# Kernel tuning notes

Hardware: AMD Instinct MI355X
Metric: run time of the kernel (lower is better)

## Reference

```python
import jax, jax.numpy as jnp
import numpy as np

NUM_HEADS = 16
HEAD_DIM = 64
DIM = NUM_HEADS * HEAD_DIM
ROPE_BASE = 10000.0
EPS = 1e-6


def rotate_half(x):
    # pairs (x0,x1) -> (-x1, x0), interleaved on last dim
    x_even = x[..., ::2]
    x_odd = x[..., 1::2]
    return jnp.stack((-x_odd, x_even), axis=-1).reshape(x.shape)


def apply_rope(q, k, positions, base=ROPE_BASE):
    d = q.shape[-1]
    inv_freq = 1.0 / (base ** (jnp.arange(0, d, 2, dtype=jnp.float32) / d))
    angles = positions.astype(jnp.float32)[..., None] * inv_freq  # [B, L, d/2]
    cos = jnp.repeat(jnp.cos(angles), 2, axis=-1).astype(q.dtype)[:, None, :, :]  # [B,1,L,d]
    sin = jnp.repeat(jnp.sin(angles), 2, axis=-1).astype(q.dtype)[:, None, :, :]
    return q * cos + rotate_half(q) * sin, k * cos + rotate_half(k) * sin


def per_head_layernorm(x, weight):
    # x: [B, H, L, d]; weight: [H, d]; bias is zeros (qkv_bias=False)
    mu = jnp.mean(x, axis=-1, keepdims=True)
    var = jnp.mean(jnp.square(x - mu), axis=-1, keepdims=True)
    xn = (x - mu) * jax.lax.rsqrt(var + EPS)
    return xn * weight[None, :, None, :]


def setup_inputs() -> dict:
    key = jax.random.key(0)
    k1, k2, k3, k4, k5 = jax.random.split(key, 5)
    B, L = 2, 2048
    x = jax.random.normal(k1, (B, L, DIM), dtype=jnp.float32)
    mask = jnp.ones((B, L, L), dtype=bool)
    positions = jnp.broadcast_to(jnp.arange(L, dtype=jnp.int64 if jax.config.jax_enable_x64 else jnp.int32), (B, L))
    s = 1.0 / np.sqrt(DIM)
    W_qkv = jax.random.normal(k2, (DIM, 3 * DIM), dtype=jnp.float32) * s
    W_out = jax.random.normal(k3, (DIM, DIM), dtype=jnp.float32) * s
    qn_w = jnp.ones((NUM_HEADS, HEAD_DIM), dtype=jnp.float32)
    kn_w = jnp.ones((NUM_HEADS, HEAD_DIM), dtype=jnp.float32)
    return {"x": x, "mask": mask, "positions": positions,
            "W_qkv": W_qkv, "W_out": W_out, "qn_w": qn_w, "kn_w": kn_w}


def reference(x, mask, positions, W_qkv, W_out, qn_w, kn_w):
    B, L, D = x.shape
    scale = HEAD_DIM ** -0.5
    qkv = x @ W_qkv  # [B, L, 3D]
    qkv = qkv.reshape(B, L, 3, NUM_HEADS, HEAD_DIM)
    qkv = jnp.transpose(qkv, (2, 0, 3, 1, 4))  # [3, B, H, L, d]
    q, k, v = qkv[0], qkv[1], qkv[2]
    q = per_head_layernorm(q, qn_w)
    k = per_head_layernorm(k, kn_w)
    q, k = apply_rope(q, k, positions)
    attn = jnp.einsum('bhqd,bhkd->bhqk', q, k) * scale  # [B, H, L, L]
    attn = jnp.where(mask[:, None, :, :], attn, -jnp.inf)
    attn = jax.nn.softmax(attn, axis=-1)
    out = jnp.einsum('bhqk,bhkd->bhqd', attn, v)  # [B, H, L, d]
    out = jnp.transpose(out, (0, 2, 1, 3)).reshape(B, L, D)
    return out @ W_out
```

## Files before the change

### kernel.cpp

```cpp
#include <hip/hip_runtime.h>


typedef __bf16 bf16x8 __attribute__((ext_vector_type(8)));
typedef __bf16 bf16x2 __attribute__((ext_vector_type(2)));
typedef float f32x4 __attribute__((ext_vector_type(4)));

#define QSCALE 0.1803368802f

__device__ __forceinline__ float bf2f(unsigned short u) {
  unsigned int v = ((unsigned int)u) << 16;
  float f;
  __builtin_memcpy(&f, &v, 4);
  return f;
}
__device__ __forceinline__ unsigned short f2bf(float f) {
  unsigned int v;
  __builtin_memcpy(&v, &f, 4);
  v += 0x7fffu + ((v >> 16) & 1u);
  return (unsigned short)(v >> 16);
}
__device__ __forceinline__ unsigned short f2bf_hw(float f) {
  __bf16 h = (__bf16)f;
  unsigned short u;
  __builtin_memcpy(&u, &h, 2);
  return u;
}
__device__ __forceinline__ unsigned int pack2(float a, float b) {
  bf16x2 t;
  t[0] = (__bf16)a;
  t[1] = (__bf16)b;
  unsigned int u;
  __builtin_memcpy(&u, &t, 4);
  return u;
}
__device__ __forceinline__ void gl_lds16(const unsigned short* g, unsigned short* l) {
  __builtin_amdgcn_global_load_lds(
      (const __attribute__((address_space(1))) unsigned int*)g,
      (__attribute__((address_space(3))) unsigned int*)l, 16, 0, 0);
}

__global__ __launch_bounds__(256) void prep(
    const float* __restrict__ x, const float* __restrict__ W_qkv,
    const float* __restrict__ W_out, const int* __restrict__ positions,
    unsigned short* __restrict__ xb,
    unsigned short* __restrict__ Wt_qkv, unsigned short* __restrict__ Wt_out,
    float2* __restrict__ lut) {
  __shared__ float tile[64][65];
  const int bid = blockIdx.x, t = threadIdx.x;
  if (bid < 4096) {
    int i = (bid * 256 + t) * 4;
    float4 v = *reinterpret_cast<const float4*>(x + i);
    ushort4 o;
    o.x = f2bf(v.x); o.y = f2bf(v.y); o.z = f2bf(v.z); o.w = f2bf(v.w);
    *reinterpret_cast<ushort4*>(xb + i) = o;
    return;
  }
  if (bid >= 5120) {
    int idx = (bid - 5120) * 256 + t;
    int m = idx >> 5, p = idx & 31;
    float pos = (float)positions[m];
    float invf = __builtin_amdgcn_exp2f(-(float)(2 * p) * (13.2877124f / 64.0f));
    float rev = pos * invf * 0.15915494f;
    rev -= floorf(rev);
    lut[idx] = make_float2(__builtin_amdgcn_cosf(rev), __builtin_amdgcn_sinf(rev));
    return;
  }
  const float* W; unsigned short* Wt; int Nd, bn, bk;
  if (bid < 4864) {
    int id = bid - 4096; W = W_qkv; Wt = Wt_qkv; Nd = 3072; bn = id % 48; bk = id / 48;
  } else {
    int id = bid - 4864; W = W_out; Wt = Wt_out; Nd = 1024; bn = id % 16; bk = id / 16;
  }
  const int Kd = 1024;
#pragma unroll
  for (int i = 0; i < 16; i++) {
    int idx = i * 256 + t;
    int k = idx >> 6, n = idx & 63;
    tile[k][n] = W[(size_t)(bk * 64 + k) * Nd + bn * 64 + n];
  }
  __syncthreads();
#pragma unroll
  for (int i = 0; i < 16; i++) {
    int idx = i * 256 + t;
    int n = idx >> 6, k = idx & 63;
    Wt[(size_t)(bn * 64 + n) * Kd + bk * 64 + k] = f2bf(tile[k][n]);
  }
}

__global__ __launch_bounds__(256, 4) void gemm_qkv(
    const unsigned short* __restrict__ A,
    const unsigned short* __restrict__ Bt,
    const float* __restrict__ qn_w, const float* __restrict__ kn_w,
    const float2* __restrict__ lut,
    unsigned short* __restrict__ Qr,
    unsigned short* __restrict__ Kr,
    unsigned short* __restrict__ Vt, int K) {
  __shared__ __align__(16) unsigned short As[2][128 * 32];
  __shared__ __align__(16) unsigned short Bs[2][128 * 32];
  const int tid = threadIdx.x;
  const int lane = tid & 63, wid = tid >> 6;
  const int quad = lane >> 4, l16 = lane & 15;
  const int wr = wid >> 1, wc = wid & 1;
  const int bn = blockIdx.x, bm = blockIdx.y;
  const unsigned short* Ab = A + (size_t)bm * 128 * K;
  const unsigned short* Bb = Bt + (size_t)bn * 128 * K;

  f32x4 acc[4][4] = {};

  const int c0 = tid, c1 = tid + 256;
  const int ar0 = c0 >> 2, ag0 = ((c0 & 3) ^ ((ar0 >> 1) & 3)) * 8;
  const int ar1 = c1 >> 2, ag1 = ((c1 & 3) ^ ((ar1 >> 1) & 3)) * 8;

  gl_lds16(Ab + (size_t)ar0 * K + ag0, &As[0][c0 * 8]);
  gl_lds16(Ab + (size_t)ar1 * K + ag1, &As[0][c1 * 8]);
  gl_lds16(Bb + (size_t)ar0 * K + ag0, &Bs[0][c0 * 8]);
  gl_lds16(Bb + (size_t)ar1 * K + ag1, &Bs[0][c1 * 8]);

  const int iters = K >> 5;
  for (int it = 0; it < iters; it++) {
    const int cur = it & 1;
    __builtin_amdgcn_s_barrier();
    if (it + 1 < iters) {
      const int k0 = (it + 1) << 5, nb = cur ^ 1;
      gl_lds16(Ab + (size_t)ar0 * K + k0 + ag0, &As[nb][c0 * 8]);
      gl_lds16(Ab + (size_t)ar1 * K + k0 + ag1, &As[nb][c1 * 8]);
      gl_lds16(Bb + (size_t)ar0 * K + k0 + ag0, &Bs[nb][c0 * 8]);
      gl_lds16(Bb + (size_t)ar1 * K + k0 + ag1, &Bs[nb][c1 * 8]);
      __builtin_amdgcn_sched_barrier(0);
      asm volatile("s_waitcnt vmcnt(4)" ::: "memory");
    } else {
      __builtin_amdgcn_sched_barrier(0);
      asm volatile("s_waitcnt vmcnt(0)" ::: "memory");
    }
    __builtin_amdgcn_sched_barrier(0);
    __builtin_amdgcn_s_setprio(1);
    const unsigned short* Ac = As[cur];
    const unsigned short* Bc = Bs[cur];
    bf16x8 af[4], bfr[4];
#pragma unroll
    for (int i = 0; i < 4; i++) {
      int m = wr * 64 + i * 16 + l16;
      af[i] = *reinterpret_cast<const bf16x8*>(&Ac[m * 32 + ((quad ^ ((m >> 1) & 3)) * 8)]);
    }
#pragma unroll
    for (int j = 0; j < 4; j++) {
      int n = wc * 64 + j * 16 + l16;
      bfr[j] = *reinterpret_cast<const bf16x8*>(&Bc[n * 32 + ((quad ^ ((n >> 1) & 3)) * 8)]);
    }
#pragma unroll
    for (int i = 0; i < 4; i++)
#pragma unroll
      for (int j = 0; j < 4; j++)
        acc[i][j] = __builtin_amdgcn_mfma_f32_16x16x32_bf16(af[i], bfr[j], acc[i][j], 0, 0, 0);
    __builtin_amdgcn_s_setprio(0);
  }

  const int sec = bn >> 3;
  const int h = (bn & 7) * 2 + wc;
  const int b = bm >> 4;
  if (sec < 2) {
    const float* gw = sec ? kn_w : qn_w;
    unsigned short* dst = sec ? Kr : Qr;
    const float oscale = sec ? 1.0f : QSCALE;
    float w4[4];
#pragma unroll
    for (int j = 0; j < 4; j++) w4[j] = gw[h * 64 + j * 16 + l16];
#pragma unroll
    for (int i = 0; i < 4; i++)
#pragma unroll
      for (int r = 0; r < 4; r++) {
        int m = bm * 128 + wr * 64 + i * 16 + quad * 4 + r;
        int l = m & 2047;
        const float2* lrow = lut + m * 32;
        float2 cs4[4];
#pragma unroll
        for (int j = 0; j < 4; j++) cs4[j] = lrow[j * 8 + (l16 >> 1)];
        float sum = acc[i][0][r] + acc[i][1][r] + acc[i][2][r] + acc[i][3][r];
        float sq = acc[i][0][r] * acc[i][0][r] + acc[i][1][r] * acc[i][1][r] +
                   acc[i][2][r] * acc[i][2][r] + acc[i][3][r] * acc[i][3][r];
#pragma unroll
        for (int off = 1; off < 16; off <<= 1) {
          sum += __shfl_xor(sum, off);
          sq += __shfl_xor(sq, off);
        }
        float mu = sum * (1.0f / 64.0f);
        float var = sq * (1.0f / 64.0f) - mu * mu;
        float rs = rsqrtf(fmaxf(var, 0.0f) + 1e-6f);
#pragma unroll
        for (int j = 0; j < 4; j++) {
          float y = (acc[i][j][r] - mu) * rs * w4[j];
          float p = __shfl_xor(y, 1);
          float o = (l16 & 1) ? (y * cs4[j].x + p * cs4[j].y)
                              : (y * cs4[j].x - p * cs4[j].y);
          dst[((size_t)(b * 16 + h) * 2048 + l) * 64 + j * 16 + l16] = f2bf(o * oscale);
        }
      }
  } else {
#pragma unroll
    for (int i = 0; i < 4; i++) {
      int lp = (bm * 128 + wr * 64 + (i >> 1) * 32 + quad * 8 + (i & 1) * 4) & 2047;
#pragma unroll
      for (int j = 0; j < 4; j++) {
        int d = j * 16 + l16;
        uint2 v;
        v.x = pack2(acc[i][j][0], acc[i][j][1]);
        v.y = pack2(acc[i][j][2], acc[i][j][3]);
        *reinterpret_cast<uint2*>(&Vt[((size_t)(b * 16 + h) * 64 + d) * 2048 + lp]) = v;
      }
    }
  }
}

__global__ __launch_bounds__(256, 2) void attn_kernel(
    const unsigned short* __restrict__ Q,
    const unsigned short* __restrict__ K,
    const unsigned short* __restrict__ Vt,
    unsigned short* __restrict__ O) {
  __shared__ __align__(16) unsigned short Ks[2][2][64 * 64];
  __shared__ __align__(16) unsigned short Vs[2][2][64 * 64];

  int bid = blockIdx.x;
  int id = (bid & 7) * 64 + (bid >> 3);
  const int qt = id & 15; id >>= 4;
  const int h = id & 15;  const int b = id >> 4;
  const int tid = threadIdx.x;
  const int lane = tid & 63, wid = tid >> 6;
  const int half = wid >> 1, wg = wid & 1;
  const int quad = lane >> 4, l16 = lane & 15;

  const unsigned short* Qb = Q + (size_t)(b * 16 + h) * 2048 * 64;
  const unsigned short* Kb = K + (size_t)(b * 16 + h) * 2048 * 64;
  const unsigned short* Vb = Vt + (size_t)(b * 16 + h) * 64 * 2048;

  const int qbase = qt * 128 + wg * 64;
  bf16x8 qf[4][2];
#pragma unroll
  for (int g = 0; g < 4; g++)
#pragma unroll
    for (int d = 0; d < 2; d++)
      qf[g][d] = *reinterpret_cast<const bf16x8*>(
          &Qb[(size_t)(qbase + g * 16 + l16) * 64 + d * 32 + quad * 8]);

  bf16x8 ones8;
#pragma unroll
  for (int i = 0; i < 8; i++) ones8[i] = (__bf16)1.0f;

  f32x4 o[4][4] = {};
  f32x4 lacc[4] = {};

  const int ltid = tid & 127;
  int cs[4], rs[4], gsw[4];
#pragma unroll
  for (int j = 0; j < 4; j++) {
    cs[j] = ltid + j * 128;
    rs[j] = cs[j] >> 3;
    gsw[j] = ((cs[j] & 7) ^ (rs[j] & 7)) * 8;
  }
  const int kb0 = half * 1024;

#pragma unroll
  for (int j = 0; j < 4; j++)
    gl_lds16(&Kb[(size_t)(kb0 + rs[j]) * 64 + gsw[j]], &Ks[half][0][cs[j] * 8]);
#pragma unroll
  for (int j = 0; j < 4; j++)
    gl_lds16(&Vb[(size_t)rs[j] * 2048 + kb0 + gsw[j]], &Vs[half][0][cs[j] * 8]);

  for (int kt = 0; kt < 16; kt++) {
    const int cur = kt & 1;
    __builtin_amdgcn_s_barrier();
    if (kt + 1 < 16) {
      const int ko = kb0 + (kt + 1) * 64, nb = cur ^ 1;
#pragma unroll
      for (int j = 0; j < 4; j++)
        gl_lds16(&Kb[(size_t)(ko + rs[j]) * 64 + gsw[j]], &Ks[half][nb][cs[j] * 8]);
#pragma unroll
      for (int j = 0; j < 4; j++)
        gl_lds16(&Vb[(size_t)rs[j] * 2048 + ko + gsw[j]], &Vs[half][nb][cs[j] * 8]);
      __builtin_amdgcn_sched_barrier(0);
      asm volatile("s_waitcnt vmcnt(8)" ::: "memory");
    } else {
      __builtin_amdgcn_sched_barrier(0);
      asm volatile("s_waitcnt vmcnt(0)" ::: "memory");
    }
    __builtin_amdgcn_sched_barrier(0);
    const unsigned short* Kc = Ks[half][cur];
    const unsigned short* Vc = Vs[half][cur];

    __builtin_amdgcn_s_setprio(1);
    f32x4 s4[4][4] = {};
#pragma unroll
    for (int kg = 0; kg < 4; kg++) {
      int row = kg * 16 + l16;
      bf16x8 kf0 = *reinterpret_cast<const bf16x8*>(
          &Kc[row * 64 + ((quad ^ (row & 7)) * 8)]);
      bf16x8 kf1 = *reinterpret_cast<const bf16x8*>(
          &Kc[row * 64 + (((4 + quad) ^ (row & 7)) * 8)]);
#pragma unroll
      for (int g = 0; g < 4; g++) {
        s4[g][kg] = __builtin_amdgcn_mfma_f32_16x16x32_bf16(kf0, qf[g][0], s4[g][kg], 0, 0, 0);
        s4[g][kg] = __builtin_amdgcn_mfma_f32_16x16x32_bf16(kf1, qf[g][1], s4[g][kg], 0, 0, 0);
      }
    }
    union u32x4v { unsigned int u[4]; bf16x8 v; };
    u32x4v pa[4][2];
#pragma unroll
    for (int g = 0; g < 4; g++) {
      float pv[4][4];
#pragma unroll
      for (int kg = 0; kg < 4; kg++)
#pragma unroll
        for (int r = 0; r < 4; r++)
          pv[kg][r] = __builtin_amdgcn_exp2f(s4[g][kg][r]);
#pragma unroll
      for (int c = 0; c < 2; c++) {
        pa[g][c].u[0] = pack2(pv[c * 2][0], pv[c * 2][1]);
        pa[g][c].u[1] = pack2(pv[c * 2][2], pv[c * 2][3]);
        pa[g][c].u[2] = pack2(pv[c * 2 + 1][0], pv[c * 2 + 1][1]);
        pa[g][c].u[3] = pack2(pv[c * 2 + 1][2], pv[c * 2 + 1][3]);
        lacc[g] = __builtin_amdgcn_mfma_f32_16x16x32_bf16(pa[g][c].v, ones8, lacc[g], 0, 0, 0);
      }
    }
#pragma unroll
    for (int c = 0; c < 2; c++)
#pragma unroll
      for (int i = 0; i < 4; i++) {
        int row = i * 16 + l16;
        bf16x8 vfr = *reinterpret_cast<const bf16x8*>(
            &Vc[row * 64 + (((c * 4 + quad) ^ (row & 7)) * 8)]);
#pragma unroll
        for (int g = 0; g < 4; g++)
          o[g][i] = __builtin_amdgcn_mfma_f32_16x16x32_bf16(pa[g][c].v, vfr, o[g][i], 0, 0, 0);
      }
    __builtin_amdgcn_s_setprio(0);
  }

  __syncthreads();
  float* Om = (float*)&Ks[0][0][0];
  float* Lm = (float*)&Vs[0][0][0];
  if (half == 0) {
#pragma unroll
    for (int g = 0; g < 4; g++) {
#pragma unroll
      for (int i = 0; i < 4; i++)
#pragma unroll
        for (int r = 0; r < 4; r++)
          Om[(wg * 64 + g * 16 + quad * 4 + r) * 64 + i * 16 + l16] = o[g][i][r];
      if (l16 == 0) {
#pragma unroll
        for (int r = 0; r < 4; r++)
          Lm[wg * 64 + g * 16 + quad * 4 + r] = lacc[g][r];
      }
    }
  }
  __syncthreads();
  if (half == 1) {
#pragma unroll
    for (int g = 0; g < 4; g++) {
#pragma unroll
      for (int r = 0; r < 4; r++) {
        float lt = lacc[g][r] + Lm[wg * 64 + g * 16 + quad * 4 + r];
        float inv = 1.0f / lt;
        int q = qbase + g * 16 + quad * 4 + r;
#pragma unroll
        for (int i = 0; i < 4; i++) {
          float sum = o[g][i][r] + Om[(wg * 64 + g * 16 + quad * 4 + r) * 64 + i * 16 + l16];
          O[((size_t)(b * 2048 + q)) * 1024 + h * 64 + i * 16 + l16] = f2bf_hw(sum * inv);
        }
      }
    }
  }
}

__global__ __launch_bounds__(256) void gemm_out(
    const unsigned short* __restrict__ A,
    const unsigned short* __restrict__ Bt,
    float* __restrict__ C, int M, int N, int K) {
  __shared__ __align__(16) unsigned short As[2][128 * 64];
  __shared__ __align__(16) unsigned short Bs[2][64 * 64];
  const int tid = threadIdx.x;
  const int lane = tid & 63, wid = tid >> 6;
  const int quad = lane >> 4, l16 = lane & 15;
  const int bn = blockIdx.x, bm = blockIdx.y;
  const unsigned short* Ab = A + (size_t)bm * 128 * K;
  const unsigned short* Bb = Bt + (size_t)bn * 64 * K;

  f32x4 acc[2][4] = {};

  int arow[4], asrc[4];
#pragma unroll
  for (int t2 = 0; t2 < 4; t2++) {
    int s = t2 * 256 + tid;
    arow[t2] = s >> 3;
    asrc[t2] = (((s & 7) ^ (arow[t2] & 7)) * 8);
  }
  int brow[2], bsrc[2];
#pragma unroll
  for (int t2 = 0; t2 < 2; t2++) {
    int s = t2 * 256 + tid;
    brow[t2] = s >> 3;
    bsrc[t2] = (((s & 7) ^ (brow[t2] & 7)) * 8);
  }

#pragma unroll
  for (int t2 = 0; t2 < 4; t2++)
    gl_lds16(Ab + (size_t)arow[t2] * K + asrc[t2], &As[0][(t2 * 256 + tid) * 8]);
#pragma unroll
  for (int t2 = 0; t2 < 2; t2++)
    gl_lds16(Bb + (size_t)brow[t2] * K + bsrc[t2], &Bs[0][(t2 * 256 + tid) * 8]);

  const int iters = K >> 6;
  for (int it = 0; it < iters; it++) {
    const int cur = it & 1;
    __builtin_amdgcn_s_barrier();
    if (it + 1 < iters) {
      const int k0 = (it + 1) << 6, nb = cur ^ 1;
#pragma unroll
      for (int t2 = 0; t2 < 4; t2++)
        gl_lds16(Ab + (size_t)arow[t2] * K + k0 + asrc[t2], &As[nb][(t2 * 256 + tid) * 8]);
#pragma unroll
      for (int t2 = 0; t2 < 2; t2++)
        gl_lds16(Bb + (size_t)brow[t2] * K + k0 + bsrc[t2], &Bs[nb][(t2 * 256 + tid) * 8]);
      __builtin_amdgcn_sched_barrier(0);
      asm volatile("s_waitcnt vmcnt(6)" ::: "memory");
    } else {
      __builtin_amdgcn_sched_barrier(0);
      asm volatile("s_waitcnt vmcnt(0)" ::: "memory");
    }
    __builtin_amdgcn_sched_barrier(0);
    __builtin_amdgcn_s_setprio(1);
    const unsigned short* Ac = As[cur];
    const unsigned short* Bc = Bs[cur];
    bf16x8 af[2][2], bfr[4][2];
#pragma unroll
    for (int i = 0; i < 2; i++) {
      int m = wid * 32 + i * 16 + l16;
#pragma unroll
      for (int kk = 0; kk < 2; kk++)
        af[i][kk] = *reinterpret_cast<const bf16x8*>(
            &Ac[(m * 8 + ((kk * 4 + quad) ^ (m & 7))) * 8]);
    }
#pragma unroll
    for (int j = 0; j < 4; j++) {
      int n = j * 16 + l16;
#pragma unroll
      for (int kk = 0; kk < 2; kk++)
        bfr[j][kk] = *reinterpret_cast<const bf16x8*>(
            &Bc[(n * 8 + ((kk * 4 + quad) ^ (n & 7))) * 8]);
    }
#pragma unroll
    for (int kk = 0; kk < 2; kk++)
#pragma unroll
      for (int i = 0; i < 2; i++)
#pragma unroll
        for (int j = 0; j < 4; j++)
          acc[i][j] = __builtin_amdgcn_mfma_f32_16x16x32_bf16(af[i][kk], bfr[j][kk], acc[i][j], 0, 0, 0);
    __builtin_amdgcn_s_setprio(0);
  }
#pragma unroll
  for (int i = 0; i < 2; i++)
#pragma unroll
    for (int j = 0; j < 4; j++)
#pragma unroll
      for (int r = 0; r < 4; r++) {
        int m = bm * 128 + wid * 32 + i * 16 + quad * 4 + r;
        int n = bn * 64 + j * 16 + l16;
        C[(size_t)m * N + n] = acc[i][j][r];
      }
}

extern "C" void kernel_launch(void* const* d_in, const int* in_sizes, int n_in,
                              void* d_out, int out_size, void* d_ws, size_t ws_size,
                              hipStream_t stream) {
  (void)in_sizes; (void)n_in; (void)out_size; (void)ws_size;
  const float* x     = (const float*)d_in[0];
  const int*   pos   = (const int*)d_in[2];
  const float* W_qkv = (const float*)d_in[3];
  const float* W_out = (const float*)d_in[4];
  const float* qn_w  = (const float*)d_in[5];
  const float* kn_w  = (const float*)d_in[6];
  float*       out   = (float*)d_out;

  char* ws = (char*)d_ws;
  unsigned short* xb     = (unsigned short*)(ws);
  unsigned short* Qr     = (unsigned short*)(ws + 8388608);
  unsigned short* Kr     = (unsigned short*)(ws + 16777216);
  unsigned short* Vt     = (unsigned short*)(ws + 25165824);
  unsigned short* Wt_qkv = (unsigned short*)(ws + 33554432);
  unsigned short* Wt_out = (unsigned short*)(ws + 39845888);
  float2*         lut    = (float2*)(ws + 41943040);
  unsigned short* attn_o = xb;

  prep<<<5632, 256, 0, stream>>>(x, W_qkv, W_out, pos, xb, Wt_qkv, Wt_out, lut);
  gemm_qkv<<<dim3(24, 32), 256, 0, stream>>>(xb, Wt_qkv, qn_w, kn_w, lut, Qr, Kr, Vt, 1024);
  attn_kernel<<<512, 256, 0, stream>>>(Qr, Kr, Vt, attn_o);
  gemm_out<<<dim3(16, 32), 256, 0, stream>>>(attn_o, Wt_out, out, 4096, 1024, 1024);
}
```

Before: 197.8 us.

## Enlarge QKV GEMM tile to 256x256 with 512 threads and K-step 64

```diff
diff --git a/kernel.cpp b/kernel.cpp
--- a/kernel.cpp
+++ b/kernel.cpp
@@ -87,7 +87,7 @@
   }
 }
 
-__global__ __launch_bounds__(256, 4) void gemm_qkv(
+__global__ __launch_bounds__(512, 2) void gemm_qkv(
     const unsigned short* __restrict__ A,
     const unsigned short* __restrict__ Bt,
     const float* __restrict__ qn_w, const float* __restrict__ kn_w,
@@ -95,39 +95,50 @@
     unsigned short* __restrict__ Qr,
     unsigned short* __restrict__ Kr,
     unsigned short* __restrict__ Vt, int K) {
-  __shared__ __align__(16) unsigned short As[2][128 * 32];
-  __shared__ __align__(16) unsigned short Bs[2][128 * 32];
+  __shared__ __align__(16) unsigned short As[2][256 * 64];
+  __shared__ __align__(16) unsigned short Bs[2][256 * 64];
   const int tid = threadIdx.x;
   const int lane = tid & 63, wid = tid >> 6;
   const int quad = lane >> 4, l16 = lane & 15;
-  const int wr = wid >> 1, wc = wid & 1;
-  const int bn = blockIdx.x, bm = blockIdx.y;
-  const unsigned short* Ab = A + (size_t)bm * 128 * K;
-  const unsigned short* Bb = Bt + (size_t)bn * 128 * K;
-
-  f32x4 acc[4][4] = {};
-
-  const int c0 = tid, c1 = tid + 256;
-  const int ar0 = c0 >> 2, ag0 = ((c0 & 3) ^ ((ar0 >> 1) & 3)) * 8;
-  const int ar1 = c1 >> 2, ag1 = ((c1 & 3) ^ ((ar1 >> 1) & 3)) * 8;
-
-  gl_lds16(Ab + (size_t)ar0 * K + ag0, &As[0][c0 * 8]);
-  gl_lds16(Ab + (size_t)ar1 * K + ag1, &As[0][c1 * 8]);
-  gl_lds16(Bb + (size_t)ar0 * K + ag0, &Bs[0][c0 * 8]);
-  gl_lds16(Bb + (size_t)ar1 * K + ag1, &Bs[0][c1 * 8]);
-
-  const int iters = K >> 5;
+  const int wr = wid >> 2, wc = wid & 3;
+  int bid = blockIdx.x;
+  int id = (bid & 7) * 24 + (bid >> 3);
+  const int bn = id >> 4;
+  const int bm = id & 15;
+  const unsigned short* Ab = A + (size_t)bm * 256 * K;
+  const unsigned short* Bb = Bt + (size_t)bn * 256 * K;
+
+  f32x4 acc[8][4] = {};
+
+  int srow[4], ssw[4];
+#pragma unroll
+  for (int t2 = 0; t2 < 4; t2++) {
+    int s = t2 * 512 + tid;
+    srow[t2] = s >> 3;
+    ssw[t2] = (((s & 7) ^ (srow[t2] & 7)) * 8);
+  }
+
+#pragma unroll
+  for (int t2 = 0; t2 < 4; t2++)
+    gl_lds16(Ab + (size_t)srow[t2] * K + ssw[t2], &As[0][(t2 * 512 + tid) * 8]);
+#pragma unroll
+  for (int t2 = 0; t2 < 4; t2++)
+    gl_lds16(Bb + (size_t)srow[t2] * K + ssw[t2], &Bs[0][(t2 * 512 + tid) * 8]);
+
+  const int iters = K >> 6;
   for (int it = 0; it < iters; it++) {
     const int cur = it & 1;
     __builtin_amdgcn_s_barrier();
     if (it + 1 < iters) {
-      const int k0 = (it + 1) << 5, nb = cur ^ 1;
-      gl_lds16(Ab + (size_t)ar0 * K + k0 + ag0, &As[nb][c0 * 8]);
-      gl_lds16(Ab + (size_t)ar1 * K + k0 + ag1, &As[nb][c1 * 8]);
-      gl_lds16(Bb + (size_t)ar0 * K + k0 + ag0, &Bs[nb][c0 * 8]);
-      gl_lds16(Bb + (size_t)ar1 * K + k0 + ag1, &Bs[nb][c1 * 8]);
+      const int k0 = (it + 1) << 6, nb = cur ^ 1;
+#pragma unroll
+      for (int t2 = 0; t2 < 4; t2++)
+        gl_lds16(Ab + (size_t)srow[t2] * K + k0 + ssw[t2], &As[nb][(t2 * 512 + tid) * 8]);
+#pragma unroll
+      for (int t2 = 0; t2 < 4; t2++)
+        gl_lds16(Bb + (size_t)srow[t2] * K + k0 + ssw[t2], &Bs[nb][(t2 * 512 + tid) * 8]);
       __builtin_amdgcn_sched_barrier(0);
-      asm volatile("s_waitcnt vmcnt(4)" ::: "memory");
+      asm volatile("s_waitcnt vmcnt(8)" ::: "memory");
     } else {
       __builtin_amdgcn_sched_barrier(0);
       asm volatile("s_waitcnt vmcnt(0)" ::: "memory");
@@ -136,28 +147,34 @@
     __builtin_amdgcn_s_setprio(1);
     const unsigned short* Ac = As[cur];
     const unsigned short* Bc = Bs[cur];
-    bf16x8 af[4], bfr[4];
-#pragma unroll
-    for (int i = 0; i < 4; i++) {
-      int m = wr * 64 + i * 16 + l16;
-      af[i] = *reinterpret_cast<const bf16x8*>(&Ac[m * 32 + ((quad ^ ((m >> 1) & 3)) * 8)]);
-    }
+    bf16x8 bfr[4][2];
 #pragma unroll
     for (int j = 0; j < 4; j++) {
       int n = wc * 64 + j * 16 + l16;
-      bfr[j] = *reinterpret_cast<const bf16x8*>(&Bc[n * 32 + ((quad ^ ((n >> 1) & 3)) * 8)]);
-    }
-#pragma unroll
-    for (int i = 0; i < 4; i++)
-#pragma unroll
-      for (int j = 0; j < 4; j++)
-        acc[i][j] = __builtin_amdgcn_mfma_f32_16x16x32_bf16(af[i], bfr[j], acc[i][j], 0, 0, 0);
+#pragma unroll
+      for (int kk = 0; kk < 2; kk++)
+        bfr[j][kk] = *reinterpret_cast<const bf16x8*>(
+            &Bc[(n * 8 + ((kk * 4 + quad) ^ (n & 7))) * 8]);
+    }
+#pragma unroll
+    for (int i = 0; i < 8; i++) {
+      int m = wr * 128 + i * 16 + l16;
+      bf16x8 af0 = *reinterpret_cast<const bf16x8*>(
+          &Ac[(m * 8 + (quad ^ (m & 7))) * 8]);
+      bf16x8 af1 = *reinterpret_cast<const bf16x8*>(
+          &Ac[(m * 8 + ((4 + quad) ^ (m & 7))) * 8]);
+#pragma unroll
+      for (int j = 0; j < 4; j++) {
+        acc[i][j] = __builtin_amdgcn_mfma_f32_16x16x32_bf16(af0, bfr[j][0], acc[i][j], 0, 0, 0);
+        acc[i][j] = __builtin_amdgcn_mfma_f32_16x16x32_bf16(af1, bfr[j][1], acc[i][j], 0, 0, 0);
+      }
+    }
     __builtin_amdgcn_s_setprio(0);
   }
 
-  const int sec = bn >> 3;
-  const int h = (bn & 7) * 2 + wc;
-  const int b = bm >> 4;
+  const int sec = bn >> 2;
+  const int h = (bn & 3) * 4 + wc;
+  const int b = bm >> 3;
   if (sec < 2) {
     const float* gw = sec ? kn_w : qn_w;
     unsigned short* dst = sec ? Kr : Qr;
@@ -166,10 +183,10 @@
 #pragma unroll
     for (int j = 0; j < 4; j++) w4[j] = gw[h * 64 + j * 16 + l16];
 #pragma unroll
-    for (int i = 0; i < 4; i++)
+    for (int i = 0; i < 8; i++)
 #pragma unroll
       for (int r = 0; r < 4; r++) {
-        int m = bm * 128 + wr * 64 + i * 16 + quad * 4 + r;
+        int m = bm * 256 + wr * 128 + i * 16 + quad * 4 + r;
         int l = m & 2047;
         const float2* lrow = lut + m * 32;
         float2 cs4[4];
@@ -197,8 +214,8 @@
       }
   } else {
 #pragma unroll
-    for (int i = 0; i < 4; i++) {
-      int lp = (bm * 128 + wr * 64 + (i >> 1) * 32 + quad * 8 + (i & 1) * 4) & 2047;
+    for (int i = 0; i < 8; i++) {
+      int lp = (bm * 256 + wr * 128 + (i >> 1) * 32 + quad * 8 + (i & 1) * 4) & 2047;
 #pragma unroll
       for (int j = 0; j < 4; j++) {
         int d = j * 16 + l16;
@@ -491,7 +508,7 @@
   unsigned short* attn_o = xb;
 
   prep<<<5632, 256, 0, stream>>>(x, W_qkv, W_out, pos, xb, Wt_qkv, Wt_out, lut);
-  gemm_qkv<<<dim3(24, 32), 256, 0, stream>>>(xb, Wt_qkv, qn_w, kn_w, lut, Qr, Kr, Vt, 1024);
+  gemm_qkv<<<192, 512, 0, stream>>>(xb, Wt_qkv, qn_w, kn_w, lut, Qr, Kr, Vt, 1024);
   attn_kernel<<<512, 256, 0, stream>>>(Qr, Kr, Vt, attn_o);
   gemm_out<<<dim3(16, 32), 256, 0, stream>>>(attn_o, Wt_out, out, 4096, 1024, 1024);
 }
```

Result: slower. 205.1 us (+3.6%).
